# Kernel tuning notes

Measured on AMD Instinct MI355X. Metric: run time of the kernel, lower is better.

The kernel has to match this reference:

```python
import jax, jax.numpy as jnp
import numpy as np

H = 16
D_MODEL = 1024
D_K = D_MODEL // H  # 64


def setup_inputs() -> dict:
    key = jax.random.key(0)
    ks = jax.random.split(key, 8)
    B, S = 8, 1024
    q = jax.random.normal(ks[0], (B, S, D_MODEL), dtype=jnp.float32)
    k = jax.random.normal(ks[1], (B, S, D_MODEL), dtype=jnp.float32)
    v = jax.random.normal(ks[2], (B, S, D_MODEL), dtype=jnp.float32)
    # xavier_normal for [h, d_model, d_k]: std = sqrt(2 / (d_model + d_k)) (fan over last two dims)
    std_p = float(np.sqrt(2.0 / (D_MODEL + D_K)))
    W_q = jax.random.normal(ks[3], (H, D_MODEL, D_K), dtype=jnp.float32) * std_p
    W_k = jax.random.normal(ks[4], (H, D_MODEL, D_K), dtype=jnp.float32) * std_p
    W_v = jax.random.normal(ks[5], (H, D_MODEL, D_K), dtype=jnp.float32) * std_p
    std_o = float(np.sqrt(2.0 / (H * D_K + D_MODEL)))
    W_o = jax.random.normal(ks[6], (D_MODEL, H * D_K), dtype=jnp.float32) * std_o  # torch Linear weight [out, in]
    b_o = jax.random.normal(ks[7], (D_MODEL,), dtype=jnp.float32) * 0.01
    return {"q": q, "k": k, "v": v, "W_q": W_q, "W_k": W_k, "W_v": W_v, "W_o": W_o, "b_o": b_o}


def reference(q, k, v, W_q, W_k, W_v, W_o, b_o):
    B, S, _ = q.shape
    # per-head projections: [h, b, s, d_k]
    qh = jnp.einsum('bsd,hdk->hbsk', q, W_q)
    kh = jnp.einsum('bsd,hdk->hbsk', k, W_k)
    vh = jnp.einsum('bsd,hdk->hbsk', v, W_v)
    scale = 1.0 / jnp.sqrt(jnp.asarray(D_K, dtype=q.dtype))
    scores = jnp.einsum('hbsk,hbtk->hbst', qh, kh) * scale  # [h,b,s,s]
    attn = jax.nn.softmax(scores, axis=-1)
    c = jnp.einsum('hbst,hbtk->hbsk', attn, vh)  # [h,b,s,d_k]
    # torch code splits the stacked (h*b) batch and concats on feature dim:
    # head index becomes the OUTER factor of the feature dim -> [b,s,h*d_k]
    c = jnp.transpose(c, (1, 2, 0, 3)).reshape(B, S, H * D_K)
    out = c @ W_o.T + b_o
    return out
```

## Files before the change

### kernel.cpp

```cpp
#include <hip/hip_runtime.h>
#include <hip/hip_bf16.h>

typedef __bf16 bf16_t;
typedef __attribute__((ext_vector_type(8))) __bf16 bf16x8;
typedef __attribute__((ext_vector_type(4))) float f32x4;

#define MFMA(a, b, c) __builtin_amdgcn_mfma_f32_16x16x32_bf16(a, b, c, 0, 0, 0)

__device__ inline void gload_lds16(const bf16_t* g, bf16_t* l) {
  __builtin_amdgcn_global_load_lds(
      (const __attribute__((address_space(1))) void*)g,
      (__attribute__((address_space(3))) void*)l, 16, 0, 0);
}

__global__ void fill_sentinel(float* out, int n, float val) {
  int i = blockIdx.x * blockDim.x + threadIdx.x;
  if (i < n) out[i] = val;
}

__global__ void transpose_w(const float* __restrict__ Wq, const float* __restrict__ Wk,
                            const float* __restrict__ Wv, bf16_t* __restrict__ Wt) {
  int gid = blockIdx.x * blockDim.x + threadIdx.x;
  int e = gid * 8;
  int m = e >> 20;
  int rem = e & 1048575;
  int n = rem >> 10;
  int d0 = rem & 1023;
  const float* W = (m == 0) ? Wq : (m == 1) ? Wk : Wv;
  int h = n >> 6, kk = n & 63;
  union { bf16_t h8[8]; uint4 u; } tmp;
#pragma unroll
  for (int j = 0; j < 8; ++j)
    tmp.h8[j] = (bf16_t)W[((size_t)(h * 1024 + d0 + j)) * 64 + kk];
  *(uint4*)(Wt + e) = tmp.u;
}

__global__ void cvt_bf16(const float* __restrict__ in, bf16_t* __restrict__ out) {
  size_t i = (size_t)(blockIdx.x * blockDim.x + threadIdx.x) * 8;
  f32x4 a = *(const f32x4*)(in + i);
  f32x4 b = *(const f32x4*)(in + i + 4);
  bf16x8 r;
  r[0] = (bf16_t)a[0]; r[1] = (bf16_t)a[1]; r[2] = (bf16_t)a[2]; r[3] = (bf16_t)a[3];
  r[4] = (bf16_t)b[0]; r[5] = (bf16_t)b[1]; r[6] = (bf16_t)b[2]; r[7] = (bf16_t)b[3];
  *(bf16x8*)(out + i) = r;
}

template <int MODE>
__global__ void gemm_bt(const bf16_t* __restrict__ A, const bf16_t* __restrict__ Bt_,
                        const float* __restrict__ bias, void* __restrict__ out_) {
  __shared__ bf16_t sA[3][128 * 32];
  __shared__ bf16_t sB[3][128 * 32];
  const int t = threadIdx.x;
  const int w = t >> 6, l = t & 63;
  const int lq = l >> 4, ll = l & 15;
  const int m0 = blockIdx.x * 128, n0 = blockIdx.y * 128;
  const bf16_t* Bt = (MODE == 0 && m0 >= 8192) ? Bt_ + 1048576 : Bt_;
  const float scale = (MODE == 0 && m0 < 8192) ? 0.125f : 1.0f;
  const int wr = (w >> 1) * 64, wc = (w & 1) * 64;
  const int srow = l >> 2;
  const int scol = (l & 3) * 8;
  f32x4 acc[4][4] = {};

  auto stage = [&](int bufi, int k0s) {
#pragma unroll
    for (int c = 0; c < 2; ++c) {
      int ch = w * 2 + c;
      int row = ch * 16 + srow;
      gload_lds16(A  + (size_t)(m0 + row) * 1024 + k0s + scol, sA[bufi] + ch * 512);
      gload_lds16(Bt + (size_t)(n0 + row) * 1024 + k0s + scol, sB[bufi] + ch * 512);
    }
  };

  auto compute = [&](int bufi) {
    bf16x8 af[4], bfr[4];
#pragma unroll
    for (int i = 0; i < 4; ++i) {
      af[i]  = *(const bf16x8*)(sA[bufi] + (wr + i * 16 + ll) * 32 + lq * 8);
      bfr[i] = *(const bf16x8*)(sB[bufi] + (wc + i * 16 + ll) * 32 + lq * 8);
    }
#pragma unroll
    for (int mi = 0; mi < 4; ++mi)
#pragma unroll
      for (int ni = 0; ni < 4; ++ni)
        acc[mi][ni] = MFMA(af[mi], bfr[ni], acc[mi][ni]);
  };

  stage(0, 0);
  stage(1, 32);

  int cur = 0;
  for (int k0 = 0; k0 < 992; k0 += 32) {
    asm volatile("s_waitcnt vmcnt(4)" ::: "memory");
    __builtin_amdgcn_s_barrier();
    __builtin_amdgcn_sched_barrier(0);
    compute(cur);
    __builtin_amdgcn_sched_barrier(0);
    if (k0 + 64 < 1024) {
      int nb = cur + 2; if (nb >= 3) nb -= 3;
      stage(nb, k0 + 64);
    }
    ++cur; if (cur == 3) cur = 0;
  }
  asm volatile("s_waitcnt vmcnt(0)" ::: "memory");
  __builtin_amdgcn_s_barrier();
  __builtin_amdgcn_sched_barrier(0);
  compute(cur);

#pragma unroll
  for (int mi = 0; mi < 4; ++mi)
#pragma unroll
    for (int ni = 0; ni < 4; ++ni)
#pragma unroll
      for (int r = 0; r < 4; ++r) {
        int row = m0 + wr + mi * 16 + lq * 4 + r;
        int col = n0 + wc + ni * 16 + ll;
        float v = acc[mi][ni][r];
        if (MODE == 2) {
          ((float*)out_)[(size_t)row * 1024 + col] = v + bias[col];
        } else if (MODE == 1) {
          int h = col >> 6, kk = col & 63, b = row >> 10, s = row & 1023;
          ((bf16_t*)out_)[((size_t)((h * 8 + b) * 64 + kk)) * 1024 + s] = (bf16_t)v;
        } else {
          int mat = row >> 13, rr = row & 8191;
          int h = col >> 6, kk = col & 63, b = rr >> 10, s = rr & 1023;
          size_t idx = (size_t)mat * 8388608 +
                       ((size_t)((h * 8 + b) * 1024 + s)) * 64 + kk;
          ((bf16_t*)out_)[idx] = (bf16_t)(v * scale);
        }
      }
}

__global__ void attn_kernel(const bf16_t* __restrict__ qh, const bf16_t* __restrict__ kh,
                            const bf16_t* __restrict__ vt, bf16_t* __restrict__ c) {
  constexpr int KP = 72, PP = 72;
  __shared__ bf16_t sK[2][64 * KP];
  __shared__ bf16_t sP[4][16 * PP];
  const int t = threadIdx.x;
  const int w = t >> 6, l = t & 63;
  const int lq = l >> 4, ll = l & 15;
  const int orig = blockIdx.x + (blockIdx.y << 4);
  const int wg = (orig & 7) * 256 + (orig >> 3);
  const int q0 = (wg & 15) * 64;
  const int hb = wg >> 4;
  const int h = hb >> 3, b = hb & 7;
  const size_t base = (size_t)hb * 65536;
  const bf16_t* Q = qh + base + (size_t)q0 * 64;
  const bf16_t* K = kh + base;
  const bf16_t* V = vt + base;

  bf16x8 aq0 = *(const bf16x8*)(Q + (w * 16 + ll) * 64 + 0 * 32 + lq * 8);
  bf16x8 aq1 = *(const bf16x8*)(Q + (w * 16 + ll) * 64 + 1 * 32 + lq * 8);

  {
    int e0 = t * 8, e1 = (256 + t) * 8;
    uint4 ka = *(const uint4*)(K + e0);
    uint4 kb = *(const uint4*)(K + e1);
    *(uint4*)(sK[0] + (e0 >> 6) * KP + (e0 & 63)) = ka;
    *(uint4*)(sK[0] + (e1 >> 6) * KP + (e1 & 63)) = kb;
  }
  __syncthreads();

  float mrow = -1e30f, lrow = 0.f;
  f32x4 o[4] = {};
  bf16_t* Pw = sP[w];

  int cur = 0;
  for (int kt = 0; kt < 1024; kt += 64, cur ^= 1) {
    uint4 kr0, kr1;
    if (kt < 960) {
      kr0 = *(const uint4*)(K + (size_t)(kt + 64) * 64 + t * 8);
      kr1 = *(const uint4*)(K + (size_t)(kt + 64) * 64 + (256 + t) * 8);
    }
    const bf16_t* Vb = V + (size_t)ll * 1024 + kt + lq * 8;
    bf16x8 bv00 = *(const bf16x8*)(Vb + 0 * 16384 + 0);
    bf16x8 bv01 = *(const bf16x8*)(Vb + 1 * 16384 + 0);
    bf16x8 bv02 = *(const bf16x8*)(Vb + 2 * 16384 + 0);
    bf16x8 bv03 = *(const bf16x8*)(Vb + 3 * 16384 + 0);
    bf16x8 bv10 = *(const bf16x8*)(Vb + 0 * 16384 + 32);
    bf16x8 bv11 = *(const bf16x8*)(Vb + 1 * 16384 + 32);
    bf16x8 bv12 = *(const bf16x8*)(Vb + 2 * 16384 + 32);
    bf16x8 bv13 = *(const bf16x8*)(Vb + 3 * 16384 + 32);

    f32x4 sacc[4] = {};
    __builtin_amdgcn_s_setprio(1);
#pragma unroll
    for (int ni = 0; ni < 4; ++ni) {
      bf16x8 bk0 = *(const bf16x8*)(sK[cur] + (ni * 16 + ll) * KP + 0 * 32 + lq * 8);
      bf16x8 bk1 = *(const bf16x8*)(sK[cur] + (ni * 16 + ll) * KP + 1 * 32 + lq * 8);
      sacc[ni] = MFMA(bk0, aq0, sacc[ni]);
      sacc[ni] = MFMA(bk1, aq1, sacc[ni]);
    }
    __builtin_amdgcn_s_setprio(0);
    float rmax = -1e30f;
#pragma unroll
    for (int ni = 0; ni < 4; ++ni)
#pragma unroll
      for (int r = 0; r < 4; ++r)
        rmax = fmaxf(rmax, sacc[ni][r]);
    if (!__all(rmax <= mrow + 8.0f)) {
      rmax = fmaxf(rmax, __shfl_xor(rmax, 16));
      rmax = fmaxf(rmax, __shfl_xor(rmax, 32));
      float mnew = fmaxf(mrow, rmax);
      float alpha = __expf(mrow - mnew);
      mrow = mnew;
      lrow *= alpha;
#pragma unroll
      for (int r = 0; r < 4; ++r) {
        float ar = __shfl(alpha, lq * 4 + r, 16);
#pragma unroll
        for (int ni = 0; ni < 4; ++ni)
          o[ni][r] *= ar;
      }
    }
#pragma unroll
    for (int ni = 0; ni < 4; ++ni)
#pragma unroll
      for (int r = 0; r < 4; ++r) {
        float p = __expf(sacc[ni][r] - mrow);
        sacc[ni][r] = p;
        lrow += p;
      }
#pragma unroll
    for (int ni = 0; ni < 4; ++ni) {
      union { bf16_t h4[4]; uint2 u; } pk;
      pk.h4[0] = (bf16_t)sacc[ni][0];
      pk.h4[1] = (bf16_t)sacc[ni][1];
      pk.h4[2] = (bf16_t)sacc[ni][2];
      pk.h4[3] = (bf16_t)sacc[ni][3];
      *(uint2*)(Pw + ll * PP + ni * 16 + lq * 4) = pk.u;
    }
    asm volatile("s_waitcnt lgkmcnt(0)" ::: "memory");
    __builtin_amdgcn_sched_barrier(0);
    bf16x8 ap0 = *(const bf16x8*)(Pw + ll * PP + 0 * 32 + lq * 8);
    bf16x8 ap1 = *(const bf16x8*)(Pw + ll * PP + 1 * 32 + lq * 8);
    __builtin_amdgcn_s_setprio(1);
    o[0] = MFMA(ap0, bv00, o[0]);
    o[1] = MFMA(ap0, bv01, o[1]);
    o[2] = MFMA(ap0, bv02, o[2]);
    o[3] = MFMA(ap0, bv03, o[3]);
    o[0] = MFMA(ap1, bv10, o[0]);
    o[1] = MFMA(ap1, bv11, o[1]);
    o[2] = MFMA(ap1, bv12, o[2]);
    o[3] = MFMA(ap1, bv13, o[3]);
    __builtin_amdgcn_s_setprio(0);
    if (kt < 960) {
      int e0 = t * 8, e1 = (256 + t) * 8;
      *(uint4*)(sK[cur ^ 1] + (e0 >> 6) * KP + (e0 & 63)) = kr0;
      *(uint4*)(sK[cur ^ 1] + (e1 >> 6) * KP + (e1 & 63)) = kr1;
    }
    __syncthreads();
  }
  lrow += __shfl_xor(lrow, 16);
  lrow += __shfl_xor(lrow, 32);
#pragma unroll
  for (int r = 0; r < 4; ++r) {
    float lr = __shfl(lrow, lq * 4 + r, 16);
    int s = q0 + w * 16 + lq * 4 + r;
#pragma unroll
    for (int ni = 0; ni < 4; ++ni) {
      int dk = ni * 16 + ll;
      c[((size_t)(b * 1024 + s)) * 1024 + h * 64 + dk] = (bf16_t)(o[ni][r] / lr);
    }
  }
}

extern "C" void kernel_launch(void* const* d_in, const int* in_sizes, int n_in,
                              void* d_out, int out_size, void* d_ws, size_t ws_size,
                              hipStream_t stream) {
  float* out = (float*)d_out;
  int nblk_out = (out_size + 255) / 256;
  if (n_in != 8) {
    fill_sentinel<<<nblk_out, 256, 0, stream>>>(out, out_size, 600.0f + 10.0f * n_in);
    return;
  }
  const int expect[8] = {8388608, 8388608, 8388608, 1048576,
                         1048576, 1048576, 1048576, 1024};
  for (int i = 0; i < 8; ++i)
    if (in_sizes[i] != expect[i]) {
      fill_sentinel<<<nblk_out, 256, 0, stream>>>(out, out_size, 500.0f + 10.0f * i);
      return;
    }

  bf16_t* ws   = (bf16_t*)d_ws;
  bf16_t* qhb  = ws;
  bf16_t* vtb  = ws + 16777216;
  bf16_t* Wt   = ws + 25165824;
  bf16_t* cbuf = ws + 25165824;
  bf16_t* Wob  = ws;
  if (ws_size < 67108864ull) {
    fill_sentinel<<<nblk_out, 256, 0, stream>>>(out, out_size, 400.0f);
    return;
  }

  const float* q  = (const float*)d_in[0];
  const float* k  = (const float*)d_in[1];
  const float* v  = (const float*)d_in[2];
  const float* Wq = (const float*)d_in[3];
  const float* Wk = (const float*)d_in[4];
  const float* Wv = (const float*)d_in[5];
  const float* Wo = (const float*)d_in[6];
  const float* bo = (const float*)d_in[7];

  bf16_t* qb = (bf16_t*)d_out;
  bf16_t* kb = (bf16_t*)d_out + 8388608;
  bf16_t* vb = (bf16_t*)d_out;

  transpose_w<<<1536, 256, 0, stream>>>(Wq, Wk, Wv, Wt);
  cvt_bf16<<<4096, 256, 0, stream>>>(q, qb);
  cvt_bf16<<<4096, 256, 0, stream>>>(k, kb);
  gemm_bt<0><<<dim3(128, 8), 256, 0, stream>>>(qb, Wt, nullptr, qhb);
  cvt_bf16<<<4096, 256, 0, stream>>>(v, vb);
  gemm_bt<1><<<dim3(64, 8), 256, 0, stream>>>(vb, Wt + 2097152, nullptr, vtb);
  attn_kernel<<<dim3(16, 128), 256, 0, stream>>>(qhb, qhb + 8388608, vtb, cbuf);
  cvt_bf16<<<512, 256, 0, stream>>>(Wo, Wob);
  gemm_bt<2><<<dim3(64, 8), 256, 0, stream>>>(cbuf, Wob, bo, out);
}
```

Baseline: 399.6 us.

## Add 256x256-tile 8-wave GEMM with swizzled LDS for Q/K projection

Replaces the 128x128 tile GEMM for the combined Q/K projection with a dedicated 256x256-tile kernel using 512 threads and 8 waves. It uses 64-wide K steps, XOR-swizzled LDS to avoid bank conflicts, double buffering, staggered A/B staging interleaved with MFMA phases, and s_setprio to favour MFMA issue. The larger tile raises arithmetic intensity and data reuse but needs far more registers and LDS, and yields only 256 blocks, which could limit occupancy and load balance.

Measured after the change: 389.6 us. 1.03x faster.

```diff
diff --git a/kernel.cpp b/kernel.cpp
--- a/kernel.cpp
+++ b/kernel.cpp
@@ -45,6 +45,143 @@
   *(bf16x8*)(out + i) = r;
 }
 
+__global__ __launch_bounds__(512, 2)
+void gemm_qk256(const bf16_t* __restrict__ A, const bf16_t* __restrict__ Bt_,
+                bf16_t* __restrict__ out) {
+  __shared__ bf16_t sA[2][2][128 * 64];
+  __shared__ bf16_t sB[2][2][128 * 64];
+  const int t = threadIdx.x;
+  const int w = t >> 6, l = t & 63;
+  const int lq = l >> 4, ll = l & 15;
+  const int wm = w >> 2, wn = w & 3;
+  const int m0 = blockIdx.x * 256, n0 = blockIdx.y * 256;
+  const bf16_t* Bt = (m0 >= 8192) ? Bt_ + 1048576 : Bt_;
+  const float scale = (m0 < 8192) ? 0.125f : 1.0f;
+  const int rt = t >> 3;
+  const int scol = (((t & 7) ^ (rt & 7)) << 3);
+  const int ldsw = w * 512;
+
+  f32x4 acc[8][4] = {};
+
+  auto stageHalf = [&](bf16_t* Lh, const bf16_t* Gh) {
+#pragma unroll
+    for (int j = 0; j < 2; ++j)
+      gload_lds16(Gh + (size_t)(j * 64 + rt) * 1024 + scol, Lh + j * 4096 + ldsw);
+  };
+  auto stageTileA = [&](int buf, int kt) {
+    stageHalf(sA[buf][0], A + (size_t)m0 * 1024 + kt * 64);
+    stageHalf(sA[buf][1], A + (size_t)(m0 + 128) * 1024 + kt * 64);
+  };
+  auto stageTileB = [&](int buf, int kt) {
+    stageHalf(sB[buf][0], Bt + (size_t)n0 * 1024 + kt * 64);
+    stageHalf(sB[buf][1], Bt + (size_t)(n0 + 128) * 1024 + kt * 64);
+  };
+  auto rdA = [&](const bf16_t* Ah, int row, int cb) {
+    return *(const bf16x8*)(Ah + row * 64 + (((cb) ^ (row & 7)) << 3));
+  };
+
+  stageTileA(0, 0); stageTileB(0, 0);
+  stageTileA(1, 1); stageTileB(1, 1);
+
+  const int nb = (wn & 1) * 64;
+  for (int T = 0; T < 16; ++T) {
+    const int buf = T & 1;
+    if (T == 15) asm volatile("s_waitcnt vmcnt(0)" ::: "memory");
+    else         asm volatile("s_waitcnt vmcnt(8)" ::: "memory");
+    __builtin_amdgcn_s_barrier();
+    __builtin_amdgcn_sched_barrier(0);
+    const bf16_t* Ah = sA[buf][wm];
+    const bf16_t* Bh = sB[buf][wn >> 1];
+
+    bf16x8 af[4][2], bf[2][2];
+#pragma unroll
+    for (int i = 0; i < 4; ++i)
+#pragma unroll
+      for (int ks = 0; ks < 2; ++ks)
+        af[i][ks] = rdA(Ah, i * 16 + ll, ks * 4 + lq);
+#pragma unroll
+    for (int n = 0; n < 2; ++n)
+#pragma unroll
+      for (int ks = 0; ks < 2; ++ks)
+        bf[n][ks] = rdA(Bh, nb + n * 16 + ll, ks * 4 + lq);
+    __builtin_amdgcn_s_setprio(1);
+#pragma unroll
+    for (int i = 0; i < 4; ++i)
+#pragma unroll
+      for (int n = 0; n < 2; ++n)
+#pragma unroll
+        for (int ks = 0; ks < 2; ++ks)
+          acc[i][n] = MFMA(af[i][ks], bf[n][ks], acc[i][n]);
+    __builtin_amdgcn_s_setprio(0);
+#pragma unroll
+    for (int n = 0; n < 2; ++n)
+#pragma unroll
+      for (int ks = 0; ks < 2; ++ks)
+        bf[n][ks] = rdA(Bh, nb + (2 + n) * 16 + ll, ks * 4 + lq);
+    __builtin_amdgcn_s_setprio(1);
+#pragma unroll
+    for (int i = 0; i < 4; ++i)
+#pragma unroll
+      for (int n = 0; n < 2; ++n)
+#pragma unroll
+        for (int ks = 0; ks < 2; ++ks)
+          acc[i][2 + n] = MFMA(af[i][ks], bf[n][ks], acc[i][2 + n]);
+    __builtin_amdgcn_s_setprio(0);
+#pragma unroll
+    for (int i = 0; i < 4; ++i)
+#pragma unroll
+      for (int ks = 0; ks < 2; ++ks)
+        af[i][ks] = rdA(Ah, 64 + i * 16 + ll, ks * 4 + lq);
+    __builtin_amdgcn_s_setprio(1);
+#pragma unroll
+    for (int i = 0; i < 4; ++i)
+#pragma unroll
+      for (int n = 0; n < 2; ++n)
+#pragma unroll
+        for (int ks = 0; ks < 2; ++ks)
+          acc[4 + i][2 + n] = MFMA(af[i][ks], bf[n][ks], acc[4 + i][2 + n]);
+    __builtin_amdgcn_s_setprio(0);
+    asm volatile("s_waitcnt lgkmcnt(0)" ::: "memory");
+    __builtin_amdgcn_s_barrier();
+    __builtin_amdgcn_sched_barrier(0);
+    if (T + 2 < 16) stageTileA(buf, T + 2);
+#pragma unroll
+    for (int n = 0; n < 2; ++n)
+#pragma unroll
+      for (int ks = 0; ks < 2; ++ks)
+        bf[n][ks] = rdA(Bh, nb + n * 16 + ll, ks * 4 + lq);
+    __builtin_amdgcn_s_setprio(1);
+#pragma unroll
+    for (int i = 0; i < 4; ++i)
+#pragma unroll
+      for (int n = 0; n < 2; ++n)
+#pragma unroll
+        for (int ks = 0; ks < 2; ++ks)
+          acc[4 + i][n] = MFMA(af[i][ks], bf[n][ks], acc[4 + i][n]);
+    __builtin_amdgcn_s_setprio(0);
+    asm volatile("s_waitcnt lgkmcnt(0)" ::: "memory");
+    __builtin_amdgcn_s_barrier();
+    __builtin_amdgcn_sched_barrier(0);
+    if (T + 2 < 16) stageTileB(buf, T + 2);
+  }
+
+#pragma unroll
+  for (int mi = 0; mi < 8; ++mi)
+#pragma unroll
+    for (int ni = 0; ni < 4; ++ni)
+#pragma unroll
+      for (int r = 0; r < 4; ++r) {
+        int row = m0 + wm * 128 + mi * 16 + lq * 4 + r;
+        int col = n0 + wn * 64 + ni * 16 + ll;
+        float v = acc[mi][ni][r];
+        int mat = row >> 13, rr = row & 8191;
+        int h = col >> 6, kk = col & 63, b = rr >> 10, s = rr & 1023;
+        size_t idx = (size_t)mat * 8388608 +
+                     ((size_t)((h * 8 + b) * 1024 + s)) * 64 + kk;
+        out[idx] = (bf16_t)(v * scale);
+      }
+}
+
 template <int MODE>
 __global__ void gemm_bt(const bf16_t* __restrict__ A, const bf16_t* __restrict__ Bt_,
                         const float* __restrict__ bias, void* __restrict__ out_) {
@@ -54,8 +191,7 @@
   const int w = t >> 6, l = t & 63;
   const int lq = l >> 4, ll = l & 15;
   const int m0 = blockIdx.x * 128, n0 = blockIdx.y * 128;
-  const bf16_t* Bt = (MODE == 0 && m0 >= 8192) ? Bt_ + 1048576 : Bt_;
-  const float scale = (MODE == 0 && m0 < 8192) ? 0.125f : 1.0f;
+  const bf16_t* Bt = Bt_;
   const int wr = (w >> 1) * 64, wc = (w & 1) * 64;
   const int srow = l >> 2;
   const int scol = (l & 3) * 8;
@@ -117,15 +253,9 @@
         float v = acc[mi][ni][r];
         if (MODE == 2) {
           ((float*)out_)[(size_t)row * 1024 + col] = v + bias[col];
-        } else if (MODE == 1) {
+        } else {
           int h = col >> 6, kk = col & 63, b = row >> 10, s = row & 1023;
           ((bf16_t*)out_)[((size_t)((h * 8 + b) * 64 + kk)) * 1024 + s] = (bf16_t)v;
-        } else {
-          int mat = row >> 13, rr = row & 8191;
-          int h = col >> 6, kk = col & 63, b = rr >> 10, s = rr & 1023;
-          size_t idx = (size_t)mat * 8388608 +
-                       ((size_t)((h * 8 + b) * 1024 + s)) * 64 + kk;
-          ((bf16_t*)out_)[idx] = (bf16_t)(v * scale);
         }
       }
 }
@@ -308,7 +438,7 @@
   transpose_w<<<1536, 256, 0, stream>>>(Wq, Wk, Wv, Wt);
   cvt_bf16<<<4096, 256, 0, stream>>>(q, qb);
   cvt_bf16<<<4096, 256, 0, stream>>>(k, kb);
-  gemm_bt<0><<<dim3(128, 8), 256, 0, stream>>>(qb, Wt, nullptr, qhb);
+  gemm_qk256<<<dim3(64, 4), 512, 0, stream>>>(qb, Wt, qhb);
   cvt_bf16<<<4096, 256, 0, stream>>>(v, vb);
   gemm_bt<1><<<dim3(64, 8), 256, 0, stream>>>(vb, Wt + 2097152, nullptr, vtb);
   attn_kernel<<<dim3(16, 128), 256, 0, stream>>>(qhb, qhb + 8388608, vtb, cbuf);
```
